# Kernel tuning notes

Hardware: AMD Instinct MI355X
Metric: run time of the kernel (lower is better)

Reference implementation:

```python
import jax, jax.numpy as jnp
import numpy as np

H = 256
NUM_REL = 460
NUM_ENT = 20000
B = 4096
CUR_TS = 10
PATH_LEN = 8


def _gru_step(x, h, W_ih, W_hh, b_ih, b_hh):
    # PyTorch GRUCell math
    gi = x @ W_ih.T + b_ih          # [B, 3H]
    gh = h @ W_hh.T + b_hh          # [B, 3H]
    ir, iz, inn = jnp.split(gi, 3, axis=1)
    hr, hz, hn = jnp.split(gh, 3, axis=1)
    r = jax.nn.sigmoid(ir + hr)
    z = jax.nn.sigmoid(iz + hz)
    n = jnp.tanh(inn + r * hn)
    return (1.0 - z) * n + z * h


def setup_inputs() -> dict:
    key = jax.random.key(0)
    ks = jax.random.split(key, 24)
    s = 1.0 / np.sqrt(H)
    f32 = jnp.float32
    d = {
        "pre_emb": jax.random.normal(ks[0], (NUM_ENT, H), f32),
        "r_emb": jax.random.normal(ks[1], (NUM_REL, H), f32),
        "partial_embeding": jax.random.normal(ks[2], (B, CUR_TS * NUM_REL), f32),
        # params (uniform-ish linear init scaled by 1/sqrt(H))
        "W_map1": jax.random.normal(ks[3], (2 * H, H), f32) * s,
        "b_map1": jax.random.normal(ks[4], (2 * H,), f32) * s,
        "W_map2": jax.random.normal(ks[5], (H, 2 * H), f32) * s,
        "b_map2": jax.random.normal(ks[6], (H,), f32) * s,
        "W_h1": jax.random.normal(ks[7], (H, H), f32) * s,
        "b_h1": jax.random.normal(ks[8], (H,), f32) * s,
        "W_h2": jax.random.normal(ks[9], (H, H), f32) * s,
        "b_h2": jax.random.normal(ks[10], (H,), f32) * s,
        "W_attn": jax.random.normal(ks[11], (H, H), f32) * s,
        "b_attn": jax.random.normal(ks[12], (H,), f32) * s,
        "W_align": jax.random.normal(ks[13], (H, H), f32) * s,
        "b_align": jax.random.normal(ks[14], (H,), f32) * s,
        "W_ih": jax.random.normal(ks[15], (3 * H, H), f32) * s,
        "W_hh": jax.random.normal(ks[16], (3 * H, H), f32) * s,
        "b_ih": jax.random.normal(ks[17], (3 * H,), f32) * s,
        "b_hh": jax.random.normal(ks[18], (3 * H,), f32) * s,
        "all_triples": jax.random.randint(ks[19], (B, 3), 0, NUM_REL, dtype=jnp.int64)
        if jax.config.jax_enable_x64 else jax.random.randint(ks[19], (B, 3), 0, NUM_REL, dtype=jnp.int32),
        "cur_ts": CUR_TS,
        "num_rel": NUM_REL,
    }
    return d


def reference(pre_emb, r_emb, partial_embeding,
              W_map1, b_map1, W_map2, b_map2,
              W_h1, b_h1, W_h2, b_h2,
              W_attn, b_attn, W_align, b_align,
              W_ih, W_hh, b_ih, b_hh,
              all_triples, cur_ts, num_rel):
    # rel_mapping1 -> rel_mapping2
    mapped_rel = (r_emb @ W_map1.T + b_map1) @ W_map2.T + b_map2     # [R, H]
    q_rel = mapped_rel[all_triples[:, 1]]                            # [B, H]

    # attention logits base (constant over timesteps): linear_attn(q_rel) @ mapped_rel.T
    attn_base = (q_rel @ W_attn.T + b_attn) @ mapped_rel.T           # [B, R]

    start_ts = max(cur_ts - PATH_LEN, 0)
    nb = partial_embeding.shape[0]
    cur_seq = partial_embeding.reshape(nb, cur_ts, num_rel)[:, start_ts:cur_ts]  # [B, T, R]
    cur_seq = jnp.swapaxes(cur_seq, 0, 1)                            # [T, B, R]

    h0 = jnp.zeros((nb, H), dtype=pre_emb.dtype)

    def step(h, cur):
        attn = cur * attn_base
        attn = jnp.where(attn == 0, jnp.asarray(-1e9, attn.dtype), attn)
        attn = jax.nn.softmax(attn, axis=1)
        x = attn @ mapped_rel                                        # [B, H]
        return _gru_step(x, h, W_ih, W_hh, b_ih, b_hh), None

    gru_hidden, _ = jax.lax.scan(step, h0, cur_seq)

    # predicted history embedding + match loss (MSE)
    predicted_hist = 0.1 * ((q_rel @ W_h1.T + b_h1) @ W_h2.T + b_h2) + q_rel
    match_loss = jnp.mean((predicted_hist - gru_hidden) ** 2)

    # forward_forth, distmult scoring
    h2 = _gru_step(q_rel, predicted_hist, W_ih, W_hh, b_ih, b_hh)    # [B, H]
    aligned_all = pre_emb @ W_align.T + b_align                      # [E, H]
    sub = aligned_all[all_triples[:, 0]]                             # [B, H]
    score_logits = (sub * h2) @ aligned_all.T                        # [B, E]
    score = jax.nn.sigmoid(score_logits)

    # BCE(sigmoid(logits), one_hot(obj)) in stable logits form without
    # materializing the dense one-hot label matrix:
    # mean over B*E of [ softplus(x) - x * label ]
    obj = all_triples[:, 2]
    pos_logits = score_logits[jnp.arange(nb), obj]
    path_loss = (jnp.sum(jax.nn.softplus(score_logits)) - jnp.sum(pos_logits)) / (nb * score_logits.shape[1])

    return match_loss, path_loss, score
```

## Files before the change

### kernel.cpp

```cpp
#include <hip/hip_runtime.h>
#include <hip/hip_bf16.h>

typedef __hip_bfloat16 bf16;
typedef __attribute__((ext_vector_type(8))) short short8;
typedef __attribute__((ext_vector_type(4))) float f32x4;
typedef __attribute__((ext_vector_type(4))) short short4v;

#define NREL 460
#define KP   480
#define NENT 20000
#define NENT_PAD 20224
#define NB   4096

__device__ inline float sigmoidf_(float x){ return 1.f/(1.f+__expf(-x)); }

__device__ inline void gload16(const bf16* g, bf16* l){
  __builtin_amdgcn_global_load_lds(
      (const __attribute__((address_space(1))) unsigned int*)g,
      (__attribute__((address_space(3))) unsigned int*)l, 16, 0, 0);
}

__device__ __forceinline__ void fgemm_body(
    const float* __restrict__ A, int lda, int arows,
    const float* __restrict__ B, int ldb,
    const float* __restrict__ bias,
    float* __restrict__ C, int ldc, int K, int mode,
    const float* __restrict__ add_src, bf16* __restrict__ ct_out,
    int bx, int by)
{
  __shared__ __align__(16) float As[32][68];
  __shared__ __align__(16) float Bs[32][68];
  const int tid = threadIdx.x;
  const int row0 = bx*64, col0 = by*64;
  const int tx = tid & 15, ty = tid >> 4;
  float acc[4][4] = {};
  for (int k0 = 0; k0 < K; k0 += 32){
    __syncthreads();
    #pragma unroll
    for (int s = 0; s < 2; ++s){
      int slot = tid + s*256;
      int r = slot >> 3, c4 = (slot & 7)*4;
      int ra = row0 + r; if (ra >= arows) ra = arows - 1;
      float4 v = *(const float4*)(A + (long)ra*lda + k0 + c4);
      As[c4+0][r] = v.x; As[c4+1][r] = v.y; As[c4+2][r] = v.z; As[c4+3][r] = v.w;
      float4 w = *(const float4*)(B + (long)(col0 + r)*ldb + k0 + c4);
      Bs[c4+0][r] = w.x; Bs[c4+1][r] = w.y; Bs[c4+2][r] = w.z; Bs[c4+3][r] = w.w;
    }
    __syncthreads();
    #pragma unroll
    for (int kk = 0; kk < 32; ++kk){
      float4 a4 = *(const float4*)(&As[kk][ty*4]);
      float4 b4 = *(const float4*)(&Bs[kk][tx*4]);
      float av[4] = {a4.x, a4.y, a4.z, a4.w};
      float bv[4] = {b4.x, b4.y, b4.z, b4.w};
      #pragma unroll
      for (int i = 0; i < 4; ++i)
        #pragma unroll
        for (int j = 0; j < 4; ++j) acc[i][j] += av[i]*bv[j];
    }
  }
  const int rb = row0 + ty*4, cb = col0 + tx*4;
  if (mode == 1){
    #pragma unroll
    for (int i = 0; i < 4; ++i){
      float4 v = {acc[i][0], acc[i][1], acc[i][2], acc[i][3]};
      *(float4*)(C + (long)(rb+i)*ldc + cb) = v;
      int rr = rb + i;
      if (rr < KP){
        #pragma unroll
        for (int j = 0; j < 4; ++j)
          ct_out[(cb+j)*KP + rr] = __float2bfloat16(rr < NREL ? acc[i][j] : 0.f);
      }
    }
  } else if (mode == 2){
    #pragma unroll
    for (int i = 0; i < 4; ++i){
      float4 v;
      #pragma unroll
      for (int j = 0; j < 4; ++j)
        ((float*)&v)[j] = 0.1f*(acc[i][j] + bias[cb+j]) + add_src[(long)(rb+i)*ldc + cb+j];
      *(float4*)(C + (long)(rb+i)*ldc + cb) = v;
    }
  } else {
    float bv[4] = {0,0,0,0};
    if (bias){ bv[0]=bias[cb]; bv[1]=bias[cb+1]; bv[2]=bias[cb+2]; bv[3]=bias[cb+3]; }
    #pragma unroll
    for (int i = 0; i < 4; ++i){
      float4 v = {acc[i][0]+bv[0], acc[i][1]+bv[1], acc[i][2]+bv[2], acc[i][3]+bv[3]};
      *(float4*)(C + (long)(rb+i)*ldc + cb) = v;
    }
  }
}

__global__ __launch_bounds__(256) void k_fgemm(
    const float* A, int lda, int arows, const float* B, int ldb,
    const float* bias, float* C, int ldc, int K, int mode,
    const float* add_src, bf16* ct_out){
  fgemm_body(A, lda, arows, B, ldb, bias, C, ldc, K, mode, add_src, ct_out,
             blockIdx.x, blockIdx.y);
}

struct FDesc {
  const float* A; const float* B; const float* bias; float* C;
  const float* add; bf16* ct;
  int lda, ldb, ldc, K, arows, mode;
};

__global__ __launch_bounds__(256) void k_fgemm_multi(FDesc d0, FDesc d1, FDesc d2,
                                                     int y1, int y2){
  int y = blockIdx.y;
  FDesc d; int by;
  if (y < y1){ d = d0; by = y; }
  else if (y < y2){ d = d1; by = y - y1; }
  else { d = d2; by = y - y2; }
  fgemm_body(d.A, d.lda, d.arows, d.B, d.ldb, d.bias, d.C, d.ldc, d.K, d.mode,
             d.add, d.ct, blockIdx.x, by);
}

__global__ __launch_bounds__(256) void k_h2(const float* __restrict__ M_ih,
    const float* __restrict__ b_ih, const float* __restrict__ ghp,
    const float* __restrict__ ph, float* __restrict__ h2_rel){
  int r = blockIdx.x, c = threadIdx.x;
  float rg = sigmoidf_(M_ih[r*768+c]       + b_ih[c]       + ghp[r*768+c]);
  float zg = sigmoidf_(M_ih[r*768+256+c]   + b_ih[256+c]   + ghp[r*768+256+c]);
  float ng = tanhf    (M_ih[r*768+512+c]   + b_ih[512+c]   + rg*ghp[r*768+512+c]);
  h2_rel[r*256+c] = (1.f - zg)*ng + zg*ph[r*256+c];
}

__global__ void k_f2bf3(const float4* __restrict__ s0, short4v* __restrict__ d0, int n0,
                        const float4* __restrict__ s1, short4v* __restrict__ d1, int n1,
                        const float4* __restrict__ s2, short4v* __restrict__ d2, int n2,
                        short4v* __restrict__ pad0, int n3, double* __restrict__ dz){
  int i = blockIdx.x*256 + threadIdx.x;
  if (i < n0+n1+n2){
    const float4* s; short4v* d; int j;
    if (i < n0){ s = s0; d = d0; j = i; }
    else if (i < n0+n1){ s = s1; d = d1; j = i-n0; }
    else { s = s2; d = d2; j = i-n0-n1; }
    float4 v = s[j];
    bf16 a = __float2bfloat16(v.x), b = __float2bfloat16(v.y);
    bf16 c = __float2bfloat16(v.z), e = __float2bfloat16(v.w);
    short4v o; o.x = *(short*)&a; o.y = *(short*)&b; o.z = *(short*)&c; o.w = *(short*)&e;
    d[j] = o;
  } else if (i < n0+n1+n2+n3){
    short4v z = {0,0,0,0};
    pad0[i - (n0+n1+n2)] = z;
  } else if (i < n0+n1+n2+n3+4){
    dz[i - (n0+n1+n2+n3)] = 0.0;
  }
}

__global__ __launch_bounds__(256) void k_soft_makep(const float* __restrict__ partial,
    const float* __restrict__ attn_base, const int* __restrict__ trips,
    bf16* __restrict__ attn_all,
    const bf16* __restrict__ Qbf, const float* __restrict__ h2_rel,
    bf16* __restrict__ P){
  int bid = blockIdx.x;
  if (bid >= NB/4){
    int i = (bid - NB/4)*256 + threadIdx.x;
    int b = i >> 8, k = i & 255;
    int s = trips[b*3+0], rel = trips[b*3+1];
    P[i] = __float2bfloat16(__bfloat162float(Qbf[s*256+k]) * h2_rel[rel*256+k]);
    return;
  }
  int wave = threadIdx.x >> 6, lane = threadIdx.x & 63;
  int b = bid*4 + wave;
  int rel = trips[b*3+1];
  const float* base = attn_base + (long)rel*512;
  float bs[8];
  #pragma unroll
  for (int s = 0; s < 8; ++s){
    int idx = s*64 + lane;
    bs[s] = (idx < NREL) ? base[idx] : 0.f;
  }
  const float* cur0 = partial + (long)b*4600 + 2*NREL;
  for (int t = 0; t < 8; ++t){
    const float* cur = cur0 + t*NREL;
    float v[8]; float mx = -1e30f;
    #pragma unroll
    for (int s = 0; s < 8; ++s){
      int idx = s*64 + lane;
      float val = -1e30f;
      if (idx < NREL){
        float pz = cur[idx]*bs[s];
        val = (pz == 0.f) ? -1e9f : pz;
      }
      v[s] = val; mx = fmaxf(mx, val);
    }
    #pragma unroll
    for (int off = 32; off >= 1; off >>= 1) mx = fmaxf(mx, __shfl_xor(mx, off));
    float sum = 0.f;
    #pragma unroll
    for (int s = 0; s < 8; ++s){
      int idx = s*64 + lane;
      if (idx < NREL){ v[s] = __expf(v[s]-mx); sum += v[s]; }
    }
    #pragma unroll
    for (int off = 32; off >= 1; off >>= 1) sum += __shfl_xor(sum, off);
    float inv = 1.f/sum;
    long obase = ((long)t*NB + b)*KP;
    #pragma unroll
    for (int s = 0; s < 8; ++s){
      int idx = s*64 + lane;
      if (idx < KP) attn_all[obase + idx] = __float2bfloat16(idx < NREL ? v[s]*inv : 0.f);
    }
  }
}

template<int MODE>
__global__ __launch_bounds__(256) void k_gemm128(
    const bf16* __restrict__ A, int lda,
    const bf16* __restrict__ B, int ldb,
    const float* __restrict__ bias,
    void* __restrict__ C, long ldc,
    int K, int n_valid, double* __restrict__ sp_sum,
    const int* __restrict__ trips)
{
  __shared__ __align__(16) bf16 sbuf[24576];
  __shared__ float wsum[8];
  const int tid = threadIdx.x;
  const int lane = tid & 63, wave = tid >> 6;
  const long row0 = (long)blockIdx.x * 128;
  const long col0 = (long)blockIdx.y * 128;
  const int sr = tid >> 2;
  const int sc = (tid & 3) * 8;
  const bf16* Ag0 = A + (row0 + sr)*lda + sc;
  const bf16* Ag1 = A + (row0 + 64 + sr)*lda + sc;
  const bf16* Bg0 = B + (col0 + sr)*ldb + sc;
  const bf16* Bg1 = B + (col0 + 64 + sr)*ldb + sc;
  bf16* As_ = sbuf;
  bf16* Bs_ = sbuf + 12288;
  const int wr = (wave >> 1)*64, wc = (wave & 1)*64;
  const int rA = lane & 15, kA = (lane >> 4)*8;
  f32x4 acc[4][4] = {};
  const int nt = K >> 5;
  auto stage = [&](int t, int buf){
    const int k0 = t << 5;
    gload16(Ag0 + k0, As_ + buf*4096 + tid*8);
    gload16(Ag1 + k0, As_ + buf*4096 + 2048 + tid*8);
    gload16(Bg0 + k0, Bs_ + buf*4096 + tid*8);
    gload16(Bg1 + k0, Bs_ + buf*4096 + 2048 + tid*8);
  };
  stage(0, 0); stage(1, 1);
  int cur = 0;
  for (int t = 0; t < nt; ++t){
    if (t + 2 < nt){
      int nb = cur + 2; if (nb >= 3) nb -= 3;
      stage(t + 2, nb);
      asm volatile("s_waitcnt vmcnt(8)" ::: "memory");
    } else if (t + 2 == nt){
      asm volatile("s_waitcnt vmcnt(4)" ::: "memory");
    } else {
      asm volatile("s_waitcnt vmcnt(0)" ::: "memory");
    }
    __builtin_amdgcn_s_barrier();
    short8 a[4], b[4];
    #pragma unroll
    for (int m = 0; m < 4; ++m) a[m] = *(const short8*)(As_ + cur*4096 + (wr + m*16 + rA)*32 + kA);
    #pragma unroll
    for (int n = 0; n < 4; ++n) b[n] = *(const short8*)(Bs_ + cur*4096 + (wc + n*16 + rA)*32 + kA);
    asm volatile("s_waitcnt lgkmcnt(0)" ::: "memory");
    __builtin_amdgcn_s_barrier();
    #pragma unroll
    for (int m = 0; m < 4; ++m)
      #pragma unroll
      for (int n = 0; n < 4; ++n)
        acc[m][n] = __builtin_amdgcn_mfma_f32_16x16x32_bf16(a[m], b[n], acc[m][n], 0,0,0);
    if (++cur == 3) cur = 0;
  }
  const int ri = (lane >> 4)*4, ci = lane & 15;
  __syncthreads();
  if constexpr (MODE == 1){
    bf16* epi = sbuf + wave*1152;
    const int rrow = lane >> 2, q = lane & 3;
    #pragma unroll
    for (int m = 0; m < 4; ++m){
      #pragma unroll
      for (int n = 0; n < 4; ++n){
        long c = col0 + wc + n*16 + ci;
        float bv = bias ? bias[c] : 0.f;
        #pragma unroll
        for (int i = 0; i < 4; ++i)
          epi[(ri+i)*72 + n*16 + ci] = __float2bfloat16(acc[m][n][i] + bv);
      }
      long gr = row0 + wr + m*16 + rrow;
      bf16* gp = (bf16*)C + gr*ldc + col0 + wc + q*16;
      const bf16* lp = epi + rrow*72 + q*16;
      *(short8*)(gp)     = *(const short8*)(lp);
      *(short8*)(gp + 8) = *(const short8*)(lp + 8);
    }
  } else {
    float* epi = (float*)sbuf + wave*1088;
    const int rrow = lane >> 2, q = lane & 3;
    const bool maybe = (col0 + wc) < 464;
    float spart = 0.f, ppart = 0.f;
    #pragma unroll
    for (int m = 0; m < 4; ++m){
      int obj[4];
      if (maybe){
        #pragma unroll
        for (int i = 0; i < 4; ++i)
          obj[i] = trips[3*(int)(row0 + wr + m*16 + ri + i) + 2];
      }
      #pragma unroll
      for (int n = 0; n < 4; ++n){
        long c = col0 + wc + n*16 + ci;
        bool cv = (c < n_valid);
        #pragma unroll
        for (int i = 0; i < 4; ++i){
          float v = acc[m][n][i];
          float sg = 0.f;
          if (cv){
            float e = __expf(-fabsf(v));
            float tt = 1.f + e;
            float rr = __builtin_amdgcn_rcpf(tt);
            sg = (v >= 0.f) ? rr : 1.f - rr;
            spart += fmaxf(v, 0.f) + e*(0.9404f - 0.2537f*e);
            if (maybe && c == obj[i]) ppart += v;
          }
          epi[(ri+i)*68 + n*16 + ci + 2] = sg;
        }
      }
      long gr = row0 + wr + m*16 + rrow;
      long c16 = col0 + wc + q*16;
      if (c16 < n_valid){
        float* gp = (float*)C + gr*ldc + c16;
        const float* lp = epi + rrow*68 + q*16 + 2;
        *(float2*)(gp)      = *(const float2*)(lp);
        *(float4*)(gp + 2)  = *(const float4*)(lp + 2);
        *(float4*)(gp + 6)  = *(const float4*)(lp + 6);
        *(float4*)(gp + 10) = *(const float4*)(lp + 10);
        *(float2*)(gp + 14) = *(const float2*)(lp + 14);
      }
    }
    #pragma unroll
    for (int off = 32; off >= 1; off >>= 1){
      spart += __shfl_xor(spart, off);
      ppart += __shfl_xor(ppart, off);
    }
    if (lane == 0){ wsum[wave] = spart; wsum[4+wave] = ppart; }
    __syncthreads();
    if (tid == 0)
      atomicAdd(sp_sum, (double)(wsum[0]+wsum[1]+wsum[2]+wsum[3]));
    if (tid == 1)
      atomicAdd(sp_sum+1, (double)(wsum[4]+wsum[5]+wsum[6]+wsum[7]));
  }
}

__global__ __launch_bounds__(512) void k_scan(
    const bf16* __restrict__ gi_all,
    const bf16* __restrict__ W_hh_bf,
    const float* __restrict__ b_hh,
    const float* __restrict__ ph,
    const int* __restrict__ trips,
    double* __restrict__ dsum)
{
  __shared__ __align__(16) bf16 hl[16*264];
  __shared__ __align__(16) bf16 gbuf[2][16*768];
  __shared__ float red[8];
  const int tid = threadIdx.x;
  const int lane = tid & 63, wave = tid >> 6;
  const int brow0 = blockIdx.x * 16;
  const int rA = lane & 15, kA = (lane >> 4) * 8;
  const int ci = lane & 15, rbase = (lane >> 4) * 4;
  float hreg[2][4] = {};
  float bh[3][2];
  #pragma unroll
  for (int f = 0; f < 2; ++f){
    int cf = wave*32 + f*16 + ci;
    bh[0][f] = b_hh[cf]; bh[1][f] = b_hh[256+cf]; bh[2][f] = b_hh[512+cf];
  }
  short8 warr[3][2][6];
  #pragma unroll
  for (int g = 0; g < 3; ++g)
    #pragma unroll
    for (int f = 0; f < 2; ++f)
      #pragma unroll
      for (int k = 0; k < 6; ++k)
        warr[g][f][k] = *(const short8*)(W_hh_bf + (g*256 + wave*32 + f*16 + rA)*256 + k*32 + kA);
  {
    const bf16* src = gi_all + (long)brow0 * 768;
    #pragma unroll
    for (int i = 0; i < 3; ++i){
      int off = (wave*3 + i)*512 + lane*8;
      gload16(src + off, gbuf[0] + off);
    }
  }
  int cur = 0;
  for (int t = 0; t < 8; ++t){
    f32x4 acc[3][2] = {};
    if (t > 0){
      #pragma unroll
      for (int k = 0; k < 8; ++k){
        short8 a = *(const short8*)(hl + rA*264 + k*32 + kA);
        #pragma unroll
        for (int g = 0; g < 3; ++g)
          #pragma unroll
          for (int f = 0; f < 2; ++f){
            short8 b;
            if (k < 6) b = warr[g][f][k];
            else b = *(const short8*)(W_hh_bf + (g*256 + wave*32 + f*16 + rA)*256 + k*32 + kA);
            acc[g][f] = __builtin_amdgcn_mfma_f32_16x16x32_bf16(a, b, acc[g][f], 0,0,0);
          }
      }
    }
    asm volatile("s_waitcnt lgkmcnt(0) vmcnt(0)" ::: "memory");
    __builtin_amdgcn_s_barrier();
    if (t < 7){
      const bf16* src = gi_all + ((long)(t+1)*NB + brow0) * 768;
      bf16* dst = gbuf[cur ^ 1];
      #pragma unroll
      for (int i = 0; i < 3; ++i){
        int off = (wave*3 + i)*512 + lane*8;
        gload16(src + off, dst + off);
      }
    }
    const bf16* gl = gbuf[cur];
    #pragma unroll
    for (int f = 0; f < 2; ++f){
      int cf = wave*32 + f*16 + ci;
      #pragma unroll
      for (int i = 0; i < 4; ++i){
        int rloc = rbase + i;
        float gir = __bfloat162float(gl[rloc*768 + cf]);
        float giz = __bfloat162float(gl[rloc*768 + 256 + cf]);
        float gin = __bfloat162float(gl[rloc*768 + 512 + cf]);
        float rg = sigmoidf_(gir + acc[0][f][i] + bh[0][f]);
        float zg = sigmoidf_(giz + acc[1][f][i] + bh[1][f]);
        float ng = tanhf(gin + rg*(acc[2][f][i] + bh[2][f]));
        float hn = (1.f - zg)*ng + zg*hreg[f][i];
        hreg[f][i] = hn;
        hl[rloc*264 + cf] = __float2bfloat16(hn);
      }
    }
    asm volatile("s_waitcnt lgkmcnt(0)" ::: "memory");
    __builtin_amdgcn_s_barrier();
    cur ^= 1;
  }
  float d = 0.f;
  #pragma unroll
  for (int f = 0; f < 2; ++f){
    int cf = wave*32 + f*16 + ci;
    #pragma unroll
    for (int i = 0; i < 4; ++i){
      int rel = trips[(brow0 + rbase + i)*3 + 1];
      float diff = ph[rel*256 + cf] - hreg[f][i];
      d += diff*diff;
    }
  }
  #pragma unroll
  for (int off = 32; off >= 1; off >>= 1) d += __shfl_xor(d, off);
  if (lane == 0) red[wave] = d;
  __syncthreads();
  if (tid == 0){
    float s = 0.f;
    #pragma unroll
    for (int w = 0; w < 8; ++w) s += red[w];
    atomicAdd(dsum, (double)s);
  }
}

__global__ void k_final(const double* __restrict__ d, float* __restrict__ out){
  out[0] = (float)(d[0] / (4096.0*256.0));
  out[1] = (float)((d[1] - d[2]) / (4096.0*20000.0));
}

extern "C" void kernel_launch(void* const* d_in, const int* in_sizes, int n_in,
                              void* d_out, int out_size, void* d_ws, size_t ws_size,
                              hipStream_t stream){
  const float* pre_emb = (const float*)d_in[0];
  const float* r_emb   = (const float*)d_in[1];
  const float* partial = (const float*)d_in[2];
  const float* W_map1  = (const float*)d_in[3];
  const float* b_map1  = (const float*)d_in[4];
  const float* W_map2  = (const float*)d_in[5];
  const float* b_map2  = (const float*)d_in[6];
  const float* W_h1    = (const float*)d_in[7];
  const float* b_h1    = (const float*)d_in[8];
  const float* W_h2    = (const float*)d_in[9];
  const float* b_h2    = (const float*)d_in[10];
  const float* W_attn  = (const float*)d_in[11];
  const float* b_attn  = (const float*)d_in[12];
  const float* W_align = (const float*)d_in[13];
  const float* b_align = (const float*)d_in[14];
  const float* W_ih    = (const float*)d_in[15];
  const float* W_hh    = (const float*)d_in[16];
  const float* b_ih    = (const float*)d_in[17];
  const float* b_hh    = (const float*)d_in[18];
  const int*   trips   = (const int*)d_in[19];
  float* out = (float*)d_out;

  char* w = (char*)d_ws;
  auto alloc = [&](size_t bytes)->char*{
    char* r = w; w += (bytes + 255) & ~size_t(255); return r;
  };
  double* dsum      = (double*)alloc(128);
  float* t1         = (float*)alloc(512*512*4);
  float* mapped     = (float*)alloc(512*256*4);
  float* a1         = (float*)alloc(512*256*4);
  float* th         = (float*)alloc(512*256*4);
  float* ph         = (float*)alloc(512*256*4);
  float* M_ih       = (float*)alloc(512*768*4);
  float* ghp        = (float*)alloc(512*768*4);
  float* attn_base  = (float*)alloc(512*512*4);
  float* h2_rel     = (float*)alloc(NREL*256*4);
  bf16*  M_ihT      = (bf16*)alloc(768*KP*2);
  bf16*  W_hh_bf    = (bf16*)alloc(768*256*2);
  bf16*  W_align_bf = (bf16*)alloc(256*256*2);
  bf16*  Q_bf       = (bf16*)alloc((size_t)NENT_PAD*256*2);
  bf16*  P_bf       = (bf16*)alloc((size_t)NB*256*2);
  bf16*  attn_all   = (bf16*)alloc((size_t)8*NB*KP*2);
  bf16*  gi_all     = (bf16*)alloc((size_t)8*NB*768*2);
  bf16*  pre_bf     = attn_all;

  {
    int n0 = NENT*256/4, n1 = 768*256/4, n2 = 256*256/4;
    int n3 = (NENT_PAD-NENT)*256/4;
    int ntot = n0+n1+n2+n3+4;
    k_f2bf3<<<(ntot+255)/256, 256, 0, stream>>>(
        (const float4*)pre_emb, (short4v*)pre_bf, n0,
        (const float4*)W_hh, (short4v*)W_hh_bf, n1,
        (const float4*)W_align, (short4v*)W_align_bf, n2,
        (short4v*)(pre_bf + (size_t)NENT*256), n3, dsum);
  }

  k_fgemm<<<dim3(8,8),256,0,stream>>>(r_emb,256,NREL, W_map1,256, b_map1, t1,512, 256, 0, nullptr, nullptr);
  k_fgemm<<<dim3(8,4),256,0,stream>>>(t1,512,512, W_map2,512, b_map2, mapped,256, 512, 0, nullptr, nullptr);
  {
    FDesc d0 = { mapped, W_ih,   nullptr, M_ih, nullptr, M_ihT, 256, 256, 768, 256, 512, 1 };
    FDesc d1 = { mapped, W_attn, b_attn,  a1,   nullptr, nullptr, 256, 256, 256, 256, 512, 0 };
    FDesc d2 = { mapped, W_h1,   b_h1,    th,   nullptr, nullptr, 256, 256, 256, 256, 512, 0 };
    k_fgemm_multi<<<dim3(8,20),256,0,stream>>>(d0, d1, d2, 12, 16);
  }
  k_fgemm<<<dim3(8,4),256,0,stream>>>(th,256,512, W_h2,256, b_h2, ph,256, 256, 2, mapped, nullptr);
  {
    FDesc d0 = { a1, mapped, nullptr, attn_base, nullptr, nullptr, 256, 256, 512, 256, 512, 0 };
    FDesc d1 = { ph, W_hh,   b_hh,    ghp,       nullptr, nullptr, 256, 256, 768, 256, 512, 0 };
    k_fgemm_multi<<<dim3(8,20),256,0,stream>>>(d0, d1, d1, 8, 20);
  }
  k_h2<<<NREL,256,0,stream>>>(M_ih, b_ih, ghp, ph, h2_rel);

  {
    dim3 g(NENT_PAD/128, 256/128);
    k_gemm128<1><<<g,256,0,stream>>>(pre_bf, 256, W_align_bf, 256, b_align,
                                     Q_bf, 256, 256, 0, nullptr, nullptr);
  }
  k_soft_makep<<<NB/4 + NB,256,0,stream>>>(partial, attn_base, trips, attn_all,
                                           Q_bf, h2_rel, P_bf);

  {
    dim3 g(8*NB/128, 768/128);
    k_gemm128<1><<<g,256,0,stream>>>(attn_all, KP, M_ihT, KP, b_ih,
                                     gi_all, 768, KP, 0, nullptr, nullptr);
  }

  k_scan<<<NB/16,512,0,stream>>>(gi_all, W_hh_bf, b_hh, ph, trips, dsum);

  {
    dim3 g(NB/128, NENT_PAD/128);
    k_gemm128<2><<<g,256,0,stream>>>(P_bf, 256, Q_bf, 256, nullptr,
                                     out+2, NENT, 256, NENT, dsum+1, trips);
  }
  k_final<<<1,1,0,stream>>>(dsum, out);
}
```

Before: 400.7 us.

## Merge independent kernels into combined launches and fold the finalize step into the scan

Several independent stages are packed into single launches that split work by block index: bf16 conversion with the first mapping GEMM, the three relation GEMMs with the entity alignment GEMM, and the score GEMM with the attention-to-gate GEMM. The h2 GRU step is recomputed inline inside the P-building kernel, and the separate finalize kernel is replaced by a last-block ticket in the scan. The intent is fewer launches and gaps between small kernels, and better occupancy from overlapping small work with large work. In exchange there is redundant GRU-gate recomputation per batch element, heterogeneous blocks sharing a shared-memory footprint sized for the larger body, and dependence on atomic ordering for the final reduction.

```diff
diff --git a/kernel.cpp b/kernel.cpp
--- a/kernel.cpp
+++ b/kernel.cpp
@@ -26,10 +26,8 @@
     const float* __restrict__ bias,
     float* __restrict__ C, int ldc, int K, int mode,
     const float* __restrict__ add_src, bf16* __restrict__ ct_out,
-    int bx, int by)
+    float* As, float* Bs, int bx, int by)
 {
-  __shared__ __align__(16) float As[32][68];
-  __shared__ __align__(16) float Bs[32][68];
   const int tid = threadIdx.x;
   const int row0 = bx*64, col0 = by*64;
   const int tx = tid & 15, ty = tid >> 4;
@@ -42,15 +40,15 @@
       int r = slot >> 3, c4 = (slot & 7)*4;
       int ra = row0 + r; if (ra >= arows) ra = arows - 1;
       float4 v = *(const float4*)(A + (long)ra*lda + k0 + c4);
-      As[c4+0][r] = v.x; As[c4+1][r] = v.y; As[c4+2][r] = v.z; As[c4+3][r] = v.w;
+      As[(c4+0)*68+r] = v.x; As[(c4+1)*68+r] = v.y; As[(c4+2)*68+r] = v.z; As[(c4+3)*68+r] = v.w;
       float4 w = *(const float4*)(B + (long)(col0 + r)*ldb + k0 + c4);
-      Bs[c4+0][r] = w.x; Bs[c4+1][r] = w.y; Bs[c4+2][r] = w.z; Bs[c4+3][r] = w.w;
+      Bs[(c4+0)*68+r] = w.x; Bs[(c4+1)*68+r] = w.y; Bs[(c4+2)*68+r] = w.z; Bs[(c4+3)*68+r] = w.w;
     }
     __syncthreads();
     #pragma unroll
     for (int kk = 0; kk < 32; ++kk){
-      float4 a4 = *(const float4*)(&As[kk][ty*4]);
-      float4 b4 = *(const float4*)(&Bs[kk][tx*4]);
+      float4 a4 = *(const float4*)(&As[kk*68 + ty*4]);
+      float4 b4 = *(const float4*)(&Bs[kk*68 + tx*4]);
       float av[4] = {a4.x, a4.y, a4.z, a4.w};
       float bv[4] = {b4.x, b4.y, b4.z, b4.w};
       #pragma unroll
@@ -92,136 +90,26 @@
   }
 }
 
-__global__ __launch_bounds__(256) void k_fgemm(
-    const float* A, int lda, int arows, const float* B, int ldb,
-    const float* bias, float* C, int ldc, int K, int mode,
-    const float* add_src, bf16* ct_out){
-  fgemm_body(A, lda, arows, B, ldb, bias, C, ldc, K, mode, add_src, ct_out,
-             blockIdx.x, blockIdx.y);
-}
-
 struct FDesc {
   const float* A; const float* B; const float* bias; float* C;
   const float* add; bf16* ct;
   int lda, ldb, ldc, K, arows, mode;
 };
 
-__global__ __launch_bounds__(256) void k_fgemm_multi(FDesc d0, FDesc d1, FDesc d2,
-                                                     int y1, int y2){
-  int y = blockIdx.y;
-  FDesc d; int by;
-  if (y < y1){ d = d0; by = y; }
-  else if (y < y2){ d = d1; by = y - y1; }
-  else { d = d2; by = y - y2; }
-  fgemm_body(d.A, d.lda, d.arows, d.B, d.ldb, d.bias, d.C, d.ldc, d.K, d.mode,
-             d.add, d.ct, blockIdx.x, by);
-}
-
-__global__ __launch_bounds__(256) void k_h2(const float* __restrict__ M_ih,
-    const float* __restrict__ b_ih, const float* __restrict__ ghp,
-    const float* __restrict__ ph, float* __restrict__ h2_rel){
-  int r = blockIdx.x, c = threadIdx.x;
-  float rg = sigmoidf_(M_ih[r*768+c]       + b_ih[c]       + ghp[r*768+c]);
-  float zg = sigmoidf_(M_ih[r*768+256+c]   + b_ih[256+c]   + ghp[r*768+256+c]);
-  float ng = tanhf    (M_ih[r*768+512+c]   + b_ih[512+c]   + rg*ghp[r*768+512+c]);
-  h2_rel[r*256+c] = (1.f - zg)*ng + zg*ph[r*256+c];
-}
-
-__global__ void k_f2bf3(const float4* __restrict__ s0, short4v* __restrict__ d0, int n0,
-                        const float4* __restrict__ s1, short4v* __restrict__ d1, int n1,
-                        const float4* __restrict__ s2, short4v* __restrict__ d2, int n2,
-                        short4v* __restrict__ pad0, int n3, double* __restrict__ dz){
-  int i = blockIdx.x*256 + threadIdx.x;
-  if (i < n0+n1+n2){
-    const float4* s; short4v* d; int j;
-    if (i < n0){ s = s0; d = d0; j = i; }
-    else if (i < n0+n1){ s = s1; d = d1; j = i-n0; }
-    else { s = s2; d = d2; j = i-n0-n1; }
-    float4 v = s[j];
-    bf16 a = __float2bfloat16(v.x), b = __float2bfloat16(v.y);
-    bf16 c = __float2bfloat16(v.z), e = __float2bfloat16(v.w);
-    short4v o; o.x = *(short*)&a; o.y = *(short*)&b; o.z = *(short*)&c; o.w = *(short*)&e;
-    d[j] = o;
-  } else if (i < n0+n1+n2+n3){
-    short4v z = {0,0,0,0};
-    pad0[i - (n0+n1+n2)] = z;
-  } else if (i < n0+n1+n2+n3+4){
-    dz[i - (n0+n1+n2+n3)] = 0.0;
-  }
-}
-
-__global__ __launch_bounds__(256) void k_soft_makep(const float* __restrict__ partial,
-    const float* __restrict__ attn_base, const int* __restrict__ trips,
-    bf16* __restrict__ attn_all,
-    const bf16* __restrict__ Qbf, const float* __restrict__ h2_rel,
-    bf16* __restrict__ P){
-  int bid = blockIdx.x;
-  if (bid >= NB/4){
-    int i = (bid - NB/4)*256 + threadIdx.x;
-    int b = i >> 8, k = i & 255;
-    int s = trips[b*3+0], rel = trips[b*3+1];
-    P[i] = __float2bfloat16(__bfloat162float(Qbf[s*256+k]) * h2_rel[rel*256+k]);
-    return;
-  }
-  int wave = threadIdx.x >> 6, lane = threadIdx.x & 63;
-  int b = bid*4 + wave;
-  int rel = trips[b*3+1];
-  const float* base = attn_base + (long)rel*512;
-  float bs[8];
-  #pragma unroll
-  for (int s = 0; s < 8; ++s){
-    int idx = s*64 + lane;
-    bs[s] = (idx < NREL) ? base[idx] : 0.f;
-  }
-  const float* cur0 = partial + (long)b*4600 + 2*NREL;
-  for (int t = 0; t < 8; ++t){
-    const float* cur = cur0 + t*NREL;
-    float v[8]; float mx = -1e30f;
-    #pragma unroll
-    for (int s = 0; s < 8; ++s){
-      int idx = s*64 + lane;
-      float val = -1e30f;
-      if (idx < NREL){
-        float pz = cur[idx]*bs[s];
-        val = (pz == 0.f) ? -1e9f : pz;
-      }
-      v[s] = val; mx = fmaxf(mx, val);
-    }
-    #pragma unroll
-    for (int off = 32; off >= 1; off >>= 1) mx = fmaxf(mx, __shfl_xor(mx, off));
-    float sum = 0.f;
-    #pragma unroll
-    for (int s = 0; s < 8; ++s){
-      int idx = s*64 + lane;
-      if (idx < NREL){ v[s] = __expf(v[s]-mx); sum += v[s]; }
-    }
-    #pragma unroll
-    for (int off = 32; off >= 1; off >>= 1) sum += __shfl_xor(sum, off);
-    float inv = 1.f/sum;
-    long obase = ((long)t*NB + b)*KP;
-    #pragma unroll
-    for (int s = 0; s < 8; ++s){
-      int idx = s*64 + lane;
-      if (idx < KP) attn_all[obase + idx] = __float2bfloat16(idx < NREL ? v[s]*inv : 0.f);
-    }
-  }
-}
-
 template<int MODE>
-__global__ __launch_bounds__(256) void k_gemm128(
+__device__ __forceinline__ void gemm128_body(
     const bf16* __restrict__ A, int lda,
     const bf16* __restrict__ B, int ldb,
     const float* __restrict__ bias,
     void* __restrict__ C, long ldc,
     int K, int n_valid, double* __restrict__ sp_sum,
-    const int* __restrict__ trips)
+    const int* __restrict__ trips,
+    bf16* sbuf, float* wsum, int bx, int by)
 {
-  __shared__ __align__(16) bf16 sbuf[24576];
-  __shared__ float wsum[8];
   const int tid = threadIdx.x;
   const int lane = tid & 63, wave = tid >> 6;
-  const long row0 = (long)blockIdx.x * 128;
-  const long col0 = (long)blockIdx.y * 128;
+  const long row0 = (long)bx * 128;
+  const long col0 = (long)by * 128;
   const int sr = tid >> 2;
   const int sc = (tid & 3) * 8;
   const bf16* Ag0 = A + (row0 + sr)*lda + sc;
@@ -347,13 +235,177 @@
   }
 }
 
+__global__ __launch_bounds__(256) void k_conv_g1(
+    const float4* __restrict__ s0, short4v* __restrict__ d0, int n0,
+    const float4* __restrict__ s1, short4v* __restrict__ d1, int n1,
+    const float4* __restrict__ s2, short4v* __restrict__ d2, int n2,
+    short4v* __restrict__ pad0, int n3, double* __restrict__ dz,
+    const float* __restrict__ gA, const float* __restrict__ gB,
+    const float* __restrict__ gbias, float* __restrict__ gC)
+{
+  __shared__ __align__(16) float As[32*68];
+  __shared__ __align__(16) float Bs[32*68];
+  int bid = blockIdx.x;
+  if (bid < 64){
+    fgemm_body(gA,256,NREL, gB,256, gbias, gC,512, 256, 0, nullptr,nullptr,
+               As, Bs, bid&7, bid>>3);
+    return;
+  }
+  int i = (bid-64)*256 + threadIdx.x;
+  if (i < n0+n1+n2){
+    const float4* s; short4v* d; int j;
+    if (i < n0){ s = s0; d = d0; j = i; }
+    else if (i < n0+n1){ s = s1; d = d1; j = i-n0; }
+    else { s = s2; d = d2; j = i-n0-n1; }
+    float4 v = s[j];
+    bf16 a = __float2bfloat16(v.x), b = __float2bfloat16(v.y);
+    bf16 c = __float2bfloat16(v.z), e = __float2bfloat16(v.w);
+    short4v o; o.x = *(short*)&a; o.y = *(short*)&b; o.z = *(short*)&c; o.w = *(short*)&e;
+    d[j] = o;
+  } else if (i < n0+n1+n2+n3){
+    short4v z = {0,0,0,0};
+    pad0[i - (n0+n1+n2)] = z;
+  } else if (i < n0+n1+n2+n3+8){
+    dz[i - (n0+n1+n2+n3)] = 0.0;
+  }
+}
+
+__global__ __launch_bounds__(256) void k_fgemm(
+    const float* A, int lda, int arows, const float* B, int ldb,
+    const float* bias, float* C, int ldc, int K, int mode,
+    const float* add_src, bf16* ct_out){
+  __shared__ __align__(16) float As[32*68];
+  __shared__ __align__(16) float Bs[32*68];
+  fgemm_body(A, lda, arows, B, ldb, bias, C, ldc, K, mode, add_src, ct_out,
+             As, Bs, blockIdx.x, blockIdx.y);
+}
+
+__global__ __launch_bounds__(256) void k_fgemm_multi(FDesc d0, FDesc d1, FDesc d2,
+                                                     int y1, int y2){
+  __shared__ __align__(16) float As[32*68];
+  __shared__ __align__(16) float Bs[32*68];
+  int y = blockIdx.y;
+  FDesc d; int by;
+  if (y < y1){ d = d0; by = y; }
+  else if (y < y2){ d = d1; by = y - y1; }
+  else { d = d2; by = y - y2; }
+  fgemm_body(d.A, d.lda, d.arows, d.B, d.ldb, d.bias, d.C, d.ldc, d.K, d.mode,
+             d.add, d.ct, As, Bs, blockIdx.x, by);
+}
+
+__global__ __launch_bounds__(256) void k_g3_aligned(
+    FDesc d0, FDesc d1, FDesc d2, int y1, int y2,
+    const bf16* __restrict__ pA, const bf16* __restrict__ pB,
+    const float* __restrict__ pbias, bf16* __restrict__ pC)
+{
+  __shared__ __align__(16) char smem[49152 + 32];
+  int bid = blockIdx.x;
+  if (bid < 160){
+    int bx = bid & 7, y = bid >> 3;
+    FDesc d; int by;
+    if (y < y1){ d = d0; by = y; }
+    else if (y < y2){ d = d1; by = y - y1; }
+    else { d = d2; by = y - y2; }
+    fgemm_body(d.A, d.lda, d.arows, d.B, d.ldb, d.bias, d.C, d.ldc, d.K, d.mode,
+               d.add, d.ct, (float*)smem, (float*)(smem + 17408), bx, by);
+  } else {
+    int idx = bid - 160;
+    gemm128_body<1>(pA, 256, pB, 256, pbias, pC, 256, 256, 0, nullptr, nullptr,
+                    (bf16*)smem, (float*)(smem + 49152), idx % 158, idx / 158);
+  }
+}
+
+__global__ __launch_bounds__(256) void k_soft_makep(const float* __restrict__ partial,
+    const float* __restrict__ attn_base, const int* __restrict__ trips,
+    bf16* __restrict__ attn_all,
+    const bf16* __restrict__ Qbf,
+    const float* __restrict__ M_ih, const float* __restrict__ ghp,
+    const float* __restrict__ ph, const float* __restrict__ b_ih,
+    bf16* __restrict__ P){
+  int bid = blockIdx.x;
+  if (bid >= NB/4){
+    int i = (bid - NB/4)*256 + threadIdx.x;
+    int b = i >> 8, k = i & 255;
+    int s = trips[b*3+0], rel = trips[b*3+1];
+    long rb = (long)rel*768;
+    float rg = sigmoidf_(M_ih[rb+k]     + b_ih[k]     + ghp[rb+k]);
+    float zg = sigmoidf_(M_ih[rb+256+k] + b_ih[256+k] + ghp[rb+256+k]);
+    float ng = tanhf    (M_ih[rb+512+k] + b_ih[512+k] + rg*ghp[rb+512+k]);
+    float h2v = (1.f - zg)*ng + zg*ph[rel*256+k];
+    P[i] = __float2bfloat16(__bfloat162float(Qbf[(long)s*256+k]) * h2v);
+    return;
+  }
+  int wave = threadIdx.x >> 6, lane = threadIdx.x & 63;
+  int b = bid*4 + wave;
+  int rel = trips[b*3+1];
+  const float* base = attn_base + (long)rel*512;
+  float bs[8];
+  #pragma unroll
+  for (int s = 0; s < 8; ++s){
+    int idx = s*64 + lane;
+    bs[s] = (idx < NREL) ? base[idx] : 0.f;
+  }
+  const float* cur0 = partial + (long)b*4600 + 2*NREL;
+  for (int t = 0; t < 8; ++t){
+    const float* cur = cur0 + t*NREL;
+    float v[8]; float mx = -1e30f;
+    #pragma unroll
+    for (int s = 0; s < 8; ++s){
+      int idx = s*64 + lane;
+      float val = -1e30f;
+      if (idx < NREL){
+        float pz = cur[idx]*bs[s];
+        val = (pz == 0.f) ? -1e9f : pz;
+      }
+      v[s] = val; mx = fmaxf(mx, val);
+    }
+    #pragma unroll
+    for (int off = 32; off >= 1; off >>= 1) mx = fmaxf(mx, __shfl_xor(mx, off));
+    float sum = 0.f;
+    #pragma unroll
+    for (int s = 0; s < 8; ++s){
+      int idx = s*64 + lane;
+      if (idx < NREL){ v[s] = __expf(v[s]-mx); sum += v[s]; }
+    }
+    #pragma unroll
+    for (int off = 32; off >= 1; off >>= 1) sum += __shfl_xor(sum, off);
+    float inv = 1.f/sum;
+    long obase = ((long)t*NB + b)*KP;
+    #pragma unroll
+    for (int s = 0; s < 8; ++s){
+      int idx = s*64 + lane;
+      if (idx < KP) attn_all[obase + idx] = __float2bfloat16(idx < NREL ? v[s]*inv : 0.f);
+    }
+  }
+}
+
+__global__ __launch_bounds__(256) void k_gemm_dual(
+    const bf16* __restrict__ A2, const bf16* __restrict__ B2,
+    void* __restrict__ C2, long ldc2, int K2, int nvalid2,
+    double* __restrict__ sp, const int* __restrict__ trips, int nblk2,
+    const bf16* __restrict__ A1, const bf16* __restrict__ B1,
+    const float* __restrict__ bias1, void* __restrict__ C1, long ldc1, int K1)
+{
+  __shared__ __align__(16) bf16 sbuf[24576];
+  __shared__ float wsum[8];
+  int bid = blockIdx.x;
+  if (bid < nblk2){
+    gemm128_body<2>(A2, 256, B2, 256, nullptr, C2, ldc2, K2, nvalid2, sp, trips,
+                    sbuf, wsum, bid & 31, bid >> 5);
+  } else {
+    int idx = bid - nblk2;
+    gemm128_body<1>(A1, KP, B1, KP, bias1, C1, ldc1, K1, 0, nullptr, nullptr,
+                    sbuf, wsum, idx & 255, idx >> 8);
+  }
+}
+
 __global__ __launch_bounds__(512) void k_scan(
     const bf16* __restrict__ gi_all,
     const bf16* __restrict__ W_hh_bf,
     const float* __restrict__ b_hh,
     const float* __restrict__ ph,
     const int* __restrict__ trips,
-    double* __restrict__ dsum)
+    double* __restrict__ dsum, int* __restrict__ done, float* __restrict__ outf)
 {
   __shared__ __align__(16) bf16 hl[16*264];
   __shared__ __align__(16) bf16 gbuf[2][16*768];
@@ -457,12 +509,16 @@
     #pragma unroll
     for (int w = 0; w < 8; ++w) s += red[w];
     atomicAdd(dsum, (double)s);
-  }
-}
-
-__global__ void k_final(const double* __restrict__ d, float* __restrict__ out){
-  out[0] = (float)(d[0] / (4096.0*256.0));
-  out[1] = (float)((d[1] - d[2]) / (4096.0*20000.0));
+    asm volatile("s_waitcnt vmcnt(0)" ::: "memory");
+    int ticket = atomicAdd(done, 1);
+    if (ticket == (int)gridDim.x - 1){
+      double m  = atomicAdd(dsum+0, 0.0);
+      double sp = atomicAdd(dsum+1, 0.0);
+      double pp = atomicAdd(dsum+2, 0.0);
+      outf[0] = (float)(m / (4096.0*256.0));
+      outf[1] = (float)((sp - pp) / (4096.0*20000.0));
+    }
+  }
 }
 
 extern "C" void kernel_launch(void* const* d_in, const int* in_sizes, int n_in,
@@ -495,6 +551,7 @@
     char* r = w; w += (bytes + 255) & ~size_t(255); return r;
   };
   double* dsum      = (double*)alloc(128);
+  int*    done      = (int*)(dsum + 4);
   float* t1         = (float*)alloc(512*512*4);
   float* mapped     = (float*)alloc(512*256*4);
   float* a1         = (float*)alloc(512*256*4);
@@ -503,7 +560,6 @@
   float* M_ih       = (float*)alloc(512*768*4);
   float* ghp        = (float*)alloc(512*768*4);
   float* attn_base  = (float*)alloc(512*512*4);
-  float* h2_rel     = (float*)alloc(NREL*256*4);
   bf16*  M_ihT      = (bf16*)alloc(768*KP*2);
   bf16*  W_hh_bf    = (bf16*)alloc(768*256*2);
   bf16*  W_align_bf = (bf16*)alloc(256*256*2);
@@ -516,50 +572,32 @@
   {
     int n0 = NENT*256/4, n1 = 768*256/4, n2 = 256*256/4;
     int n3 = (NENT_PAD-NENT)*256/4;
-    int ntot = n0+n1+n2+n3+4;
-    k_f2bf3<<<(ntot+255)/256, 256, 0, stream>>>(
+    int ntot = n0+n1+n2+n3+8;
+    k_conv_g1<<<64 + (ntot+255)/256, 256, 0, stream>>>(
         (const float4*)pre_emb, (short4v*)pre_bf, n0,
         (const float4*)W_hh, (short4v*)W_hh_bf, n1,
         (const float4*)W_align, (short4v*)W_align_bf, n2,
-        (short4v*)(pre_bf + (size_t)NENT*256), n3, dsum);
-  }
-
-  k_fgemm<<<dim3(8,8),256,0,stream>>>(r_emb,256,NREL, W_map1,256, b_map1, t1,512, 256, 0, nullptr, nullptr);
+        (short4v*)(pre_bf + (size_t)NENT*256), n3, dsum,
+        r_emb, W_map1, b_map1, t1);
+  }
   k_fgemm<<<dim3(8,4),256,0,stream>>>(t1,512,512, W_map2,512, b_map2, mapped,256, 512, 0, nullptr, nullptr);
   {
     FDesc d0 = { mapped, W_ih,   nullptr, M_ih, nullptr, M_ihT, 256, 256, 768, 256, 512, 1 };
     FDesc d1 = { mapped, W_attn, b_attn,  a1,   nullptr, nullptr, 256, 256, 256, 256, 512, 0 };
     FDesc d2 = { mapped, W_h1,   b_h1,    th,   nullptr, nullptr, 256, 256, 256, 256, 512, 0 };
-    k_fgemm_multi<<<dim3(8,20),256,0,stream>>>(d0, d1, d2, 12, 16);
-  }
-  k_fgemm<<<dim3(8,4),256,0,stream>>>(th,256,512, W_h2,256, b_h2, ph,256, 256, 2, mapped, nullptr);
+    k_g3_aligned<<<160 + 316, 256, 0, stream>>>(d0, d1, d2, 12, 16,
+                                                pre_bf, W_align_bf, b_align, Q_bf);
+  }
   {
-    FDesc d0 = { a1, mapped, nullptr, attn_base, nullptr, nullptr, 256, 256, 512, 256, 512, 0 };
-    FDesc d1 = { ph, W_hh,   b_hh,    ghp,       nullptr, nullptr, 256, 256, 768, 256, 512, 0 };
-    k_fgemm_multi<<<dim3(8,20),256,0,stream>>>(d0, d1, d1, 8, 20);
-  }
-  k_h2<<<NREL,256,0,stream>>>(M_ih, b_ih, ghp, ph, h2_rel);
-
-  {
-    dim3 g(NENT_PAD/128, 256/128);
-    k_gemm128<1><<<g,256,0,stream>>>(pre_bf, 256, W_align_bf, 256, b_align,
-                                     Q_bf, 256, 256, 0, nullptr, nullptr);
-  }
+    FDesc d0 = { th, W_h2,   b_h2,    ph,        mapped,  nullptr, 256, 256, 256, 256, 512, 2 };
+    FDesc d1 = { a1, mapped, nullptr, attn_base, nullptr, nullptr, 256, 256, 512, 256, 512, 0 };
+    k_fgemm_multi<<<dim3(8,12),256,0,stream>>>(d0, d1, d1, 4, 12);
+  }
+  k_fgemm<<<dim3(8,12),256,0,stream>>>(ph,256,512, W_hh,256, b_hh, ghp,768, 256, 0, nullptr, nullptr);
   k_soft_makep<<<NB/4 + NB,256,0,stream>>>(partial, attn_base, trips, attn_all,
-                                           Q_bf, h2_rel, P_bf);
-
-  {
-    dim3 g(8*NB/128, 768/128);
-    k_gemm128<1><<<g,256,0,stream>>>(attn_all, KP, M_ihT, KP, b_ih,
-                                     gi_all, 768, KP, 0, nullptr, nullptr);
-  }
-
-  k_scan<<<NB/16,512,0,stream>>>(gi_all, W_hh_bf, b_hh, ph, trips, dsum);
-
-  {
-    dim3 g(NB/128, NENT_PAD/128);
-    k_gemm128<2><<<g,256,0,stream>>>(P_bf, 256, Q_bf, 256, nullptr,
-                                     out+2, NENT, 256, NENT, dsum+1, trips);
-  }
-  k_final<<<1,1,0,stream>>>(dsum, out);
-}
+                                           Q_bf, M_ih, ghp, ph, b_ih, P_bf);
+  k_gemm_dual<<<5056 + 1536, 256, 0, stream>>>(
+      P_bf, Q_bf, out+2, NENT, 256, NENT, dsum+1, trips, 5056,
+      attn_all, M_ihT, b_ih, gi_all, 768, KP);
+  k_scan<<<NB/16,512,0,stream>>>(gi_all, W_hh_bf, b_hh, ph, trips, dsum, done, out);
+}
```

Result: faster. 391.0 us (-2.4%).
